# Kernel tuning notes

Measured on AMD Instinct MI355X. Metric: run time of the kernel, lower is better.

## Reference

```python
import jax, jax.numpy as jnp
import numpy as np

N = 100000
E = 1600000
D_IN = 128
D_H = 128
D_OUT = 128
LN_EPS = 1e-5
NORM_EPS = 1e-12


def _sage_conv(x, src, dst, Wl, bl, Wr):
    # PyG SAGEConv(mean): out = lin_l(mean_{j in N(i)} x_j) + lin_r(x_i)
    msgs = x[src]                                             # [E, d] gather
    summed = jax.ops.segment_sum(msgs, dst, num_segments=N)   # [N, d]
    cnt = jax.ops.segment_sum(jnp.ones((src.shape[0],), x.dtype), dst, num_segments=N)
    mean = summed / jnp.maximum(cnt, 1.0)[:, None]
    return mean @ Wl + bl + x @ Wr


def _layer_norm(x, g, b):
    mu = jnp.mean(x, axis=-1, keepdims=True)
    var = jnp.mean(jnp.square(x - mu), axis=-1, keepdims=True)
    return (x - mu) * jax.lax.rsqrt(var + LN_EPS) * g + b


def setup_inputs() -> dict:
    key = jax.random.key(0)
    ks = jax.random.split(key, 20)
    x = jax.random.normal(ks[0], (N, D_IN), dtype=jnp.float32)
    edge_index = jax.random.randint(ks[1], (2, E), 0, N, dtype=jnp.int64)
    dims = [(D_IN, D_H), (D_H, D_H), (D_H, D_OUT)]
    inp = {"x": x, "edge_index": edge_index}
    for i, (di, do) in enumerate(dims):
        s = 1.0 / np.sqrt(di)
        inp[f"Wl{i}"] = jax.random.normal(ks[2 + 5 * i], (di, do), dtype=jnp.float32) * s
        inp[f"bl{i}"] = jnp.zeros((do,), dtype=jnp.float32)
        inp[f"Wr{i}"] = jax.random.normal(ks[3 + 5 * i], (di, do), dtype=jnp.float32) * s
        inp[f"g{i}"] = jnp.ones((do,), dtype=jnp.float32)
        inp[f"b{i}"] = jnp.zeros((do,), dtype=jnp.float32)
    return inp


def reference(x, edge_index, Wl0, bl0, Wr0, g0, b0, Wl1, bl1, Wr1, g1, b1, Wl2, bl2, Wr2, g2, b2):
    src, dst = edge_index[0], edge_index[1]
    params = [(Wl0, bl0, Wr0, g0, b0), (Wl1, bl1, Wr1, g1, b1), (Wl2, bl2, Wr2, g2, b2)]
    h = x
    for i, (Wl, bl, Wr, g, b) in enumerate(params):
        h = _sage_conv(h, src, dst, Wl, bl, Wr)
        h = _layer_norm(h, g, b)
        if i < len(params) - 1:
            h = jax.nn.elu(h)
            # dropout is identity in eval mode
    # F.normalize(p=2, dim=-1)
    nrm = jnp.sqrt(jnp.sum(jnp.square(h), axis=-1, keepdims=True))
    return h / jnp.maximum(nrm, NORM_EPS)
```

## Files before the change

kernel.cpp:

```cpp
#include <hip/hip_runtime.h>
#include <hip/hip_bf16.h>
#include <math.h>

#define N_NODES 100000
#define N_EDGES 1600000
#define D 128
#define NB 391
#define BSTRIDE 6000

#define OFF_SSRC 0
#define OFF_OFFS 6400000
#define OFF_PACK 6800016
#define OFF_GC   7193232
#define OFF_BB   7195296
#define OFF_M    7204112
#define OFF_XHI  58404112
#define OFF_XLO  84004112

typedef __attribute__((ext_vector_type(8))) short short8;
typedef __attribute__((ext_vector_type(4))) float floatx4;

__device__ __forceinline__ unsigned short f2bf(float f) {
    unsigned int u = __float_as_uint(f);
    u += 0x7fffu + ((u >> 16) & 1u);
    return (unsigned short)(u >> 16);
}
__device__ __forceinline__ float bf2f(unsigned short h) {
    return __uint_as_float(((unsigned int)h) << 16);
}

__global__ __launch_bounds__(256) void part_kernel(const int* __restrict__ src,
                                                   const int* __restrict__ dst,
                                                   int* __restrict__ gcur,
                                                   uint2* __restrict__ staging) {
    __shared__ int hist[NB];
    __shared__ int base[NB];
    int t = threadIdx.x;
    int e0 = blockIdx.x * 4096;
    for (int i = t; i < NB; i += 256) hist[i] = 0;
    __syncthreads();
    int d[16];
#pragma unroll
    for (int i = 0; i < 16; ++i) {
        int e = e0 + i * 256 + t;
        d[i] = (e < N_EDGES) ? dst[e] : -1;
        if (d[i] >= 0) atomicAdd(&hist[d[i] >> 8], 1);
    }
    __syncthreads();
    for (int i = t; i < NB; i += 256) {
        int h = hist[i];
        base[i] = h ? atomicAdd(&gcur[i], h) : 0;
    }
    __syncthreads();
    for (int i = t; i < NB; i += 256) hist[i] = 0;
    __syncthreads();
#pragma unroll
    for (int i = 0; i < 16; ++i) {
        if (d[i] >= 0) {
            int e = e0 + i * 256 + t;
            int b = d[i] >> 8;
            int slot = atomicAdd(&hist[b], 1);
            staging[b * BSTRIDE + base[b] + slot] =
                make_uint2((unsigned)src[e], (unsigned)(d[i] & 255));
        }
    }
}

__global__ void bscan_kernel(const int* __restrict__ gcur, int* __restrict__ bbase,
                             int* __restrict__ offs) {
    __shared__ int sh[512];
    int t = threadIdx.x;
    int v = (t < NB) ? gcur[t] : 0;
    sh[t] = v;
    __syncthreads();
    for (int off = 1; off < 512; off <<= 1) {
        int y = (t >= off) ? sh[t - off] : 0;
        __syncthreads();
        sh[t] += y;
        __syncthreads();
    }
    if (t < NB) bbase[t] = sh[t] - v;
    if (t == 0) offs[N_NODES] = N_EDGES;
}

__global__ __launch_bounds__(256) void bsort_kernel(const uint2* __restrict__ staging,
                                                    const int* __restrict__ gcur,
                                                    const int* __restrict__ bbase,
                                                    int* __restrict__ offs,
                                                    int* __restrict__ s_src) {
    __shared__ int cnt[256];
    __shared__ int scn[256];
    __shared__ int ssrc[BSTRIDE];
    int b = blockIdx.x;
    int t = threadIdx.x;
    int n = gcur[b];
    int base_out = bbase[b];
    cnt[t] = 0;
    __syncthreads();
    for (int e = t; e < n; e += 256) {
        uint2 v = staging[b * BSTRIDE + e];
        atomicAdd(&cnt[v.y], 1);
    }
    __syncthreads();
    int v = cnt[t];
    scn[t] = v;
    __syncthreads();
    for (int off = 1; off < 256; off <<= 1) {
        int y = (t >= off) ? scn[t - off] : 0;
        __syncthreads();
        scn[t] += y;
        __syncthreads();
    }
    int ex = scn[t] - v;
    int node = b * 256 + t;
    if (node < N_NODES) offs[node] = base_out + ex;
    cnt[t] = ex;
    __syncthreads();
    for (int e = t; e < n; e += 256) {
        uint2 w = staging[b * BSTRIDE + e];
        int slot = atomicAdd(&cnt[w.y], 1);
        ssrc[slot] = (int)w.x;
    }
    __syncthreads();
    for (int e = t; e < n; e += 256) s_src[base_out + e] = ssrc[e];
}

__global__ void pack_kernel(const float* __restrict__ Wl0, const float* __restrict__ Wr0,
                            const float* __restrict__ Wl1, const float* __restrict__ Wr1,
                            const float* __restrict__ Wl2, const float* __restrict__ Wr2,
                            unsigned short* __restrict__ pack) {
    int tid = blockIdx.x * blockDim.x + threadIdx.x;
    int l = tid >> 15;
    int r = tid & 32767;
    int k = r >> 7;
    int n = r & 127;
    const float* Wl = (l == 0) ? Wl0 : (l == 1) ? Wl1 : Wl2;
    const float* Wr = (l == 0) ? Wr0 : (l == 1) ? Wr1 : Wr2;
    float v = (k < 128) ? Wl[k * 128 + n] : Wr[(k - 128) * 128 + n];
    unsigned short hi = f2bf(v);
    unsigned short lo = f2bf(v - bf2f(hi));
    int ct = n >> 4, ks = k >> 5, lane = ((k >> 3) & 3) * 16 + (n & 15), j = k & 7;
    int idx = ((ct * 8 + ks) * 64 + lane) * 8 + j;
    pack[l * 65536 + idx] = hi;
    pack[l * 65536 + 32768 + idx] = lo;
}

__global__ __launch_bounds__(256) void cvt_kernel(const float* __restrict__ x,
                                                  unsigned int* __restrict__ Xhi,
                                                  unsigned int* __restrict__ Xlo) {
    int i = blockIdx.x * 256 + threadIdx.x;
    float2 v = ((const float2*)x)[i];
    unsigned short h0 = f2bf(v.x), h1 = f2bf(v.y);
    unsigned short l0 = f2bf(v.x - bf2f(h0)), l1 = f2bf(v.y - bf2f(h1));
    Xhi[i] = (unsigned int)h0 | ((unsigned int)h1 << 16);
    Xlo[i] = (unsigned int)l0 | ((unsigned int)l1 << 16);
}

__global__ __launch_bounds__(128, 5) void fused_kernel(const uint4* __restrict__ X4,
                                                       const unsigned short* __restrict__ Xh,
                                                       const unsigned short* __restrict__ Xl,
                                                       unsigned short* __restrict__ XhO,
                                                       unsigned short* __restrict__ XlO,
                                                       const int* __restrict__ s_src,
                                                       const int* __restrict__ offs,
                                                       const unsigned short* __restrict__ packh,
                                                       const unsigned short* __restrict__ packl,
                                                       const float* __restrict__ bl,
                                                       const float* __restrict__ g,
                                                       const float* __restrict__ b,
                                                       float* __restrict__ outf, int last) {
    __shared__ float lmean[32 * 128];
    int t = threadIdx.x;
    int wid = t >> 6, lane = t & 63;
    int sub = lane >> 4, li = lane & 15;
    int nodebase = blockIdx.x * 32;

    int off_l = offs[min(nodebase + wid * 16 + min(lane, 16), N_NODES)];

#define ACC_U4(u)                                                                  \
    do {                                                                           \
        const unsigned int w_[4] = {(u).x, (u).y, (u).z, (u).w};                   \
        _Pragma("unroll") for (int j_ = 0; j_ < 4; ++j_) {                         \
            acc[2 * j_]     += bf2f((unsigned short)w_[j_]);                       \
            acc[2 * j_ + 1] += bf2f((unsigned short)(w_[j_] >> 16));               \
        }                                                                          \
    } while (0)

    for (int i = 0; i < 16; ++i) {
        int lrow = wid * 16 + i;
        int beg = __shfl(off_l, i);
        int end = __shfl(off_l, i + 1);
        int deg = end - beg;
        float acc[8];
#pragma unroll
        for (int j = 0; j < 8; ++j) acc[j] = 0.f;

        for (int cbase = 0; cbase < deg; cbase += 64) {
            int cnt = min(deg - cbase, 64);
            int myidx = s_src[min(beg + cbase + lane, N_EDGES - 1)];
            int j = 0;
            for (; j + 16 <= cnt; j += 16) {
                int i0 = __shfl(myidx, j + sub);
                int i1 = __shfl(myidx, j + 4 + sub);
                int i2 = __shfl(myidx, j + 8 + sub);
                int i3 = __shfl(myidx, j + 12 + sub);
                uint4 u0 = X4[i0 * 16 + li];
                uint4 u1 = X4[i1 * 16 + li];
                uint4 u2 = X4[i2 * 16 + li];
                uint4 u3 = X4[i3 * 16 + li];
                ACC_U4(u0); ACC_U4(u1); ACC_U4(u2); ACC_U4(u3);
            }
            if (j + 8 <= cnt) {
                int i0 = __shfl(myidx, j + sub);
                int i1 = __shfl(myidx, j + 4 + sub);
                uint4 u0 = X4[i0 * 16 + li];
                uint4 u1 = X4[i1 * 16 + li];
                ACC_U4(u0); ACC_U4(u1);
                j += 8;
            }
            if (j + 4 <= cnt) {
                int i0 = __shfl(myidx, j + sub);
                uint4 u0 = X4[i0 * 16 + li];
                ACC_U4(u0);
                j += 4;
            }
            int rem = cnt - j;
            if (rem > 0) {
                int i0 = __shfl(myidx, j + min(sub, rem - 1));
                uint4 u0 = X4[i0 * 16 + li];
                if (sub < rem) ACC_U4(u0);
            }
        }
#pragma unroll
        for (int j = 0; j < 8; ++j) {
            acc[j] += __shfl_xor(acc[j], 16);
            acc[j] += __shfl_xor(acc[j], 32);
        }
        float inv = 1.0f / fmaxf((float)deg, 1.0f);
        if (sub < 2) {
            int chunk = li * 2 + sub;
            floatx4 v = {acc[sub * 4] * inv, acc[sub * 4 + 1] * inv,
                         acc[sub * 4 + 2] * inv, acc[sub * 4 + 3] * inv};
            *(floatx4*)&lmean[lrow * 128 + ((chunk ^ (lrow & 7)) << 2)] = v;
        }
    }
#undef ACC_U4

    int colb = lane & 15;
    int quad = lane >> 4;
    int kq = quad * 8;
    int tilebase = nodebase + wid * 16;

    int rowA = min(tilebase + colb, N_NODES - 1);
    int lrowA = wid * 16 + colb;
    int rsalt = lrowA & 7;

    floatx4 acc[8];
#pragma unroll
    for (int ct = 0; ct < 8; ++ct) acc[ct] = (floatx4){0.f, 0.f, 0.f, 0.f};

#pragma unroll
    for (int ks = 0; ks < 4; ++ks) {
        int chunk0 = ks * 8 + quad * 2;
        short8 ah, al;
        {
            floatx4 v0 = *(const floatx4*)&lmean[lrowA * 128 + ((chunk0 ^ rsalt) << 2)];
            floatx4 v1 = *(const floatx4*)&lmean[lrowA * 128 + (((chunk0 + 1) ^ rsalt) << 2)];
            float v[8] = {v0[0], v0[1], v0[2], v0[3], v1[0], v1[1], v1[2], v1[3]};
#pragma unroll
            for (int j = 0; j < 8; ++j) {
                unsigned short hi = f2bf(v[j]);
                ah[j] = (short)hi;
                al[j] = (short)f2bf(v[j] - bf2f(hi));
            }
        }
#pragma unroll
        for (int ct = 0; ct < 8; ++ct) {
            int fo = ((ct * 8 + ks) << 9) + (lane << 3);
            short8 bh = *(const short8*)(packh + fo);
            short8 bo = *(const short8*)(packl + fo);
            acc[ct] = __builtin_amdgcn_mfma_f32_16x16x32_bf16(ah, bh, acc[ct], 0, 0, 0);
            acc[ct] = __builtin_amdgcn_mfma_f32_16x16x32_bf16(al, bh, acc[ct], 0, 0, 0);
            acc[ct] = __builtin_amdgcn_mfma_f32_16x16x32_bf16(ah, bo, acc[ct], 0, 0, 0);
        }
    }
#pragma unroll
    for (int ks = 4; ks < 8; ++ks) {
        int kof = (ks - 4) * 32 + kq;
        long o = (long)rowA * D + kof;
        short8 ah = *(const short8*)(Xh + o);
        short8 al = *(const short8*)(Xl + o);
#pragma unroll
        for (int ct = 0; ct < 8; ++ct) {
            int fo = ((ct * 8 + ks) << 9) + (lane << 3);
            short8 bh = *(const short8*)(packh + fo);
            short8 bo = *(const short8*)(packl + fo);
            acc[ct] = __builtin_amdgcn_mfma_f32_16x16x32_bf16(ah, bh, acc[ct], 0, 0, 0);
            acc[ct] = __builtin_amdgcn_mfma_f32_16x16x32_bf16(al, bh, acc[ct], 0, 0, 0);
            acc[ct] = __builtin_amdgcn_mfma_f32_16x16x32_bf16(ah, bo, acc[ct], 0, 0, 0);
        }
    }

    float bb[8], gg[8], b2[8];
#pragma unroll
    for (int ct = 0; ct < 8; ++ct) {
        bb[ct] = bl[ct * 16 + colb];
        gg[ct] = g[ct * 16 + colb];
        b2[ct] = b[ct * 16 + colb];
    }

#pragma unroll
    for (int ct = 0; ct < 8; ++ct)
#pragma unroll
        for (int e = 0; e < 4; ++e) acc[ct][e] += bb[ct];
    float mu[4], rstd[4];
#pragma unroll
    for (int e = 0; e < 4; ++e) {
        float s = 0.f;
#pragma unroll
        for (int ct = 0; ct < 8; ++ct) s += acc[ct][e];
        s += __shfl_xor(s, 1); s += __shfl_xor(s, 2);
        s += __shfl_xor(s, 4); s += __shfl_xor(s, 8);
        mu[e] = s * (1.0f / 128.0f);
    }
#pragma unroll
    for (int e = 0; e < 4; ++e) {
        float q = 0.f;
#pragma unroll
        for (int ct = 0; ct < 8; ++ct) {
            float d = acc[ct][e] - mu[e];
            q += d * d;
        }
        q += __shfl_xor(q, 1); q += __shfl_xor(q, 2);
        q += __shfl_xor(q, 4); q += __shfl_xor(q, 8);
        rstd[e] = rsqrtf(q * (1.0f / 128.0f) + 1e-5f);
    }
#pragma unroll
    for (int ct = 0; ct < 8; ++ct)
#pragma unroll
        for (int e = 0; e < 4; ++e) {
            float y = (acc[ct][e] - mu[e]) * rstd[e] * gg[ct] + b2[ct];
            if (!last) y = (y > 0.f) ? y : expm1f(y);
            acc[ct][e] = y;
        }
    if (last) {
#pragma unroll
        for (int e = 0; e < 4; ++e) {
            float ss = 0.f;
#pragma unroll
            for (int ct = 0; ct < 8; ++ct) {
                float y = acc[ct][e];
                ss += y * y;
            }
            ss += __shfl_xor(ss, 1); ss += __shfl_xor(ss, 2);
            ss += __shfl_xor(ss, 4); ss += __shfl_xor(ss, 8);
            float inv = 1.0f / fmaxf(sqrtf(ss), 1e-12f);
#pragma unroll
            for (int ct = 0; ct < 8; ++ct) acc[ct][e] *= inv;
        }
#pragma unroll
        for (int e = 0; e < 4; ++e) {
            int row = tilebase + quad * 4 + e;
            if (row < N_NODES) {
#pragma unroll
                for (int ct = 0; ct < 8; ++ct)
                    outf[(long)row * D + ct * 16 + colb] = acc[ct][e];
            }
        }
    } else {
#pragma unroll
        for (int e = 0; e < 4; ++e) {
            int row = tilebase + quad * 4 + e;
            if (row < N_NODES) {
#pragma unroll
                for (int ct = 0; ct < 8; ++ct) {
                    float y = acc[ct][e];
                    unsigned short hh = f2bf(y);
                    unsigned short ll = f2bf(y - bf2f(hh));
                    long o = (long)row * D + ct * 16 + colb;
                    XhO[o] = hh;
                    XlO[o] = ll;
                }
            }
        }
    }
}

extern "C" void kernel_launch(void* const* d_in, const int* in_sizes, int n_in,
                              void* d_out, int out_size, void* d_ws, size_t ws_size,
                              hipStream_t stream) {
    const float* x = (const float*)d_in[0];
    const int* edges = (const int*)d_in[1];
    const int* src = edges;
    const int* dst = edges + N_EDGES;
    const float* Wl[3] = {(const float*)d_in[2], (const float*)d_in[7],  (const float*)d_in[12]};
    const float* bl[3] = {(const float*)d_in[3], (const float*)d_in[8],  (const float*)d_in[13]};
    const float* Wr[3] = {(const float*)d_in[4], (const float*)d_in[9],  (const float*)d_in[14]};
    const float* g[3]  = {(const float*)d_in[5], (const float*)d_in[10], (const float*)d_in[15]};
    const float* b[3]  = {(const float*)d_in[6], (const float*)d_in[11], (const float*)d_in[16]};

    char* ws = (char*)d_ws;
    int* s_src = (int*)(ws + OFF_SSRC);
    int* offs  = (int*)(ws + OFF_OFFS);
    unsigned short* wpack = (unsigned short*)(ws + OFF_PACK);
    int* gcur  = (int*)(ws + OFF_GC);
    int* bbase = (int*)(ws + OFF_BB);
    uint2* staging = (uint2*)(ws + OFF_M);
    unsigned short* XhB = (unsigned short*)(ws + OFF_M);
    unsigned short* XlB = (unsigned short*)(ws + OFF_M + 25600000);
    unsigned short* XhA = (unsigned short*)(ws + OFF_XHI);
    unsigned short* XlA = (unsigned short*)(ws + OFF_XLO);
    float* out = (float*)d_out;

    hipMemsetAsync(gcur, 0, NB * sizeof(int), stream);
    part_kernel<<<(N_EDGES + 4095) / 4096, 256, 0, stream>>>(src, dst, gcur, staging);
    bscan_kernel<<<1, 512, 0, stream>>>(gcur, bbase, offs);
    bsort_kernel<<<NB, 256, 0, stream>>>(staging, gcur, bbase, offs, s_src);
    pack_kernel<<<(3 * 32768) / 256, 256, 0, stream>>>(Wl[0], Wr[0], Wl[1], Wr[1], Wl[2], Wr[2], wpack);
    cvt_kernel<<<(N_NODES * 64) / 256, 256, 0, stream>>>(x, (unsigned int*)XhA, (unsigned int*)XlA);

    const int FB = (N_NODES + 31) / 32;
    unsigned short* ph[3] = {wpack, wpack + 65536, wpack + 131072};

    fused_kernel<<<FB, 128, 0, stream>>>((const uint4*)XhA, XhA, XlA, XhB, XlB,
                                         s_src, offs, ph[0], ph[0] + 32768,
                                         bl[0], g[0], b[0], nullptr, 0);
    fused_kernel<<<FB, 128, 0, stream>>>((const uint4*)XhB, XhB, XlB, XhA, XlA,
                                         s_src, offs, ph[1], ph[1] + 32768,
                                         bl[1], g[1], b[1], nullptr, 0);
    fused_kernel<<<FB, 128, 0, stream>>>((const uint4*)XhA, XhA, XlA, nullptr, nullptr,
                                         s_src, offs, ph[2], ph[2] + 32768,
                                         bl[2], g[2], b[2], out, 1);
}
```

Baseline: 593.2 us.

## Merge partition, weight pack and convert kernels; pack staging entries into one word

```diff
diff --git a/kernel.cpp b/kernel.cpp
--- a/kernel.cpp
+++ b/kernel.cpp
@@ -29,40 +29,72 @@
     return __uint_as_float(((unsigned int)h) << 16);
 }
 
-__global__ __launch_bounds__(256) void part_kernel(const int* __restrict__ src,
+__global__ __launch_bounds__(256) void prep_kernel(const int* __restrict__ src,
                                                    const int* __restrict__ dst,
                                                    int* __restrict__ gcur,
-                                                   uint2* __restrict__ staging) {
-    __shared__ int hist[NB];
-    __shared__ int base[NB];
+                                                   unsigned int* __restrict__ staging,
+                                                   const float* __restrict__ Wl0, const float* __restrict__ Wr0,
+                                                   const float* __restrict__ Wl1, const float* __restrict__ Wr1,
+                                                   const float* __restrict__ Wl2, const float* __restrict__ Wr2,
+                                                   unsigned short* __restrict__ wpack,
+                                                   const float* __restrict__ x,
+                                                   unsigned int* __restrict__ Xhi,
+                                                   unsigned int* __restrict__ Xlo) {
+    int bid = blockIdx.x;
     int t = threadIdx.x;
-    int e0 = blockIdx.x * 4096;
-    for (int i = t; i < NB; i += 256) hist[i] = 0;
-    __syncthreads();
-    int d[16];
-#pragma unroll
-    for (int i = 0; i < 16; ++i) {
-        int e = e0 + i * 256 + t;
-        d[i] = (e < N_EDGES) ? dst[e] : -1;
-        if (d[i] >= 0) atomicAdd(&hist[d[i] >> 8], 1);
-    }
-    __syncthreads();
-    for (int i = t; i < NB; i += 256) {
-        int h = hist[i];
-        base[i] = h ? atomicAdd(&gcur[i], h) : 0;
-    }
-    __syncthreads();
-    for (int i = t; i < NB; i += 256) hist[i] = 0;
-    __syncthreads();
-#pragma unroll
-    for (int i = 0; i < 16; ++i) {
-        if (d[i] >= 0) {
+    if (bid < NB) {
+        __shared__ int hist[NB];
+        __shared__ int base[NB];
+        int e0 = bid * 4096;
+        for (int i = t; i < NB; i += 256) hist[i] = 0;
+        __syncthreads();
+        int d[16];
+#pragma unroll
+        for (int i = 0; i < 16; ++i) {
             int e = e0 + i * 256 + t;
-            int b = d[i] >> 8;
-            int slot = atomicAdd(&hist[b], 1);
-            staging[b * BSTRIDE + base[b] + slot] =
-                make_uint2((unsigned)src[e], (unsigned)(d[i] & 255));
-        }
+            d[i] = (e < N_EDGES) ? dst[e] : -1;
+            if (d[i] >= 0) atomicAdd(&hist[d[i] >> 8], 1);
+        }
+        __syncthreads();
+        for (int i = t; i < NB; i += 256) {
+            int h = hist[i];
+            base[i] = h ? atomicAdd(&gcur[i], h) : 0;
+        }
+        __syncthreads();
+        for (int i = t; i < NB; i += 256) hist[i] = 0;
+        __syncthreads();
+#pragma unroll
+        for (int i = 0; i < 16; ++i) {
+            if (d[i] >= 0) {
+                int e = e0 + i * 256 + t;
+                int b = d[i] >> 8;
+                int slot = atomicAdd(&hist[b], 1);
+                staging[b * BSTRIDE + base[b] + slot] =
+                    ((unsigned int)src[e] << 8) | (unsigned int)(d[i] & 255);
+            }
+        }
+    } else if (bid < NB + 384) {
+        int tid = (bid - NB) * 256 + t;
+        int l = tid >> 15;
+        int r = tid & 32767;
+        int k = r >> 7;
+        int n = r & 127;
+        const float* Wl = (l == 0) ? Wl0 : (l == 1) ? Wl1 : Wl2;
+        const float* Wr = (l == 0) ? Wr0 : (l == 1) ? Wr1 : Wr2;
+        float v = (k < 128) ? Wl[k * 128 + n] : Wr[(k - 128) * 128 + n];
+        unsigned short hi = f2bf(v);
+        unsigned short lo = f2bf(v - bf2f(hi));
+        int ct = n >> 4, ks = k >> 5, lane = ((k >> 3) & 3) * 16 + (n & 15), j = k & 7;
+        int idx = ((ct * 8 + ks) * 64 + lane) * 8 + j;
+        wpack[l * 65536 + idx] = hi;
+        wpack[l * 65536 + 32768 + idx] = lo;
+    } else {
+        int i = (bid - NB - 384) * 256 + t;
+        float2 v = ((const float2*)x)[i];
+        unsigned short h0 = f2bf(v.x), h1 = f2bf(v.y);
+        unsigned short l0 = f2bf(v.x - bf2f(h0)), l1 = f2bf(v.y - bf2f(h1));
+        Xhi[i] = (unsigned int)h0 | ((unsigned int)h1 << 16);
+        Xlo[i] = (unsigned int)l0 | ((unsigned int)l1 << 16);
     }
 }
 
@@ -83,11 +115,11 @@
     if (t == 0) offs[N_NODES] = N_EDGES;
 }
 
-__global__ __launch_bounds__(256) void bsort_kernel(const uint2* __restrict__ staging,
-                                                    const int* __restrict__ gcur,
-                                                    const int* __restrict__ bbase,
-                                                    int* __restrict__ offs,
-                                                    int* __restrict__ s_src) {
+__global__ __launch_bounds__(1024) void bsort_kernel(const unsigned int* __restrict__ staging,
+                                                     const int* __restrict__ gcur,
+                                                     const int* __restrict__ bbase,
+                                                     int* __restrict__ offs,
+                                                     int* __restrict__ s_src) {
     __shared__ int cnt[256];
     __shared__ int scn[256];
     __shared__ int ssrc[BSTRIDE];
@@ -95,65 +127,35 @@
     int t = threadIdx.x;
     int n = gcur[b];
     int base_out = bbase[b];
-    cnt[t] = 0;
-    __syncthreads();
-    for (int e = t; e < n; e += 256) {
-        uint2 v = staging[b * BSTRIDE + e];
-        atomicAdd(&cnt[v.y], 1);
-    }
-    __syncthreads();
-    int v = cnt[t];
-    scn[t] = v;
+    if (t < 256) cnt[t] = 0;
+    __syncthreads();
+    for (int e = t; e < n; e += 1024)
+        atomicAdd(&cnt[staging[b * BSTRIDE + e] & 255u], 1);
+    __syncthreads();
+    int v = 0;
+    if (t < 256) { v = cnt[t]; scn[t] = v; }
     __syncthreads();
     for (int off = 1; off < 256; off <<= 1) {
-        int y = (t >= off) ? scn[t - off] : 0;
-        __syncthreads();
-        scn[t] += y;
-        __syncthreads();
-    }
-    int ex = scn[t] - v;
-    int node = b * 256 + t;
-    if (node < N_NODES) offs[node] = base_out + ex;
-    cnt[t] = ex;
-    __syncthreads();
-    for (int e = t; e < n; e += 256) {
-        uint2 w = staging[b * BSTRIDE + e];
-        int slot = atomicAdd(&cnt[w.y], 1);
-        ssrc[slot] = (int)w.x;
-    }
-    __syncthreads();
-    for (int e = t; e < n; e += 256) s_src[base_out + e] = ssrc[e];
-}
-
-__global__ void pack_kernel(const float* __restrict__ Wl0, const float* __restrict__ Wr0,
-                            const float* __restrict__ Wl1, const float* __restrict__ Wr1,
-                            const float* __restrict__ Wl2, const float* __restrict__ Wr2,
-                            unsigned short* __restrict__ pack) {
-    int tid = blockIdx.x * blockDim.x + threadIdx.x;
-    int l = tid >> 15;
-    int r = tid & 32767;
-    int k = r >> 7;
-    int n = r & 127;
-    const float* Wl = (l == 0) ? Wl0 : (l == 1) ? Wl1 : Wl2;
-    const float* Wr = (l == 0) ? Wr0 : (l == 1) ? Wr1 : Wr2;
-    float v = (k < 128) ? Wl[k * 128 + n] : Wr[(k - 128) * 128 + n];
-    unsigned short hi = f2bf(v);
-    unsigned short lo = f2bf(v - bf2f(hi));
-    int ct = n >> 4, ks = k >> 5, lane = ((k >> 3) & 3) * 16 + (n & 15), j = k & 7;
-    int idx = ((ct * 8 + ks) * 64 + lane) * 8 + j;
-    pack[l * 65536 + idx] = hi;
-    pack[l * 65536 + 32768 + idx] = lo;
-}
-
-__global__ __launch_bounds__(256) void cvt_kernel(const float* __restrict__ x,
-                                                  unsigned int* __restrict__ Xhi,
-                                                  unsigned int* __restrict__ Xlo) {
-    int i = blockIdx.x * 256 + threadIdx.x;
-    float2 v = ((const float2*)x)[i];
-    unsigned short h0 = f2bf(v.x), h1 = f2bf(v.y);
-    unsigned short l0 = f2bf(v.x - bf2f(h0)), l1 = f2bf(v.y - bf2f(h1));
-    Xhi[i] = (unsigned int)h0 | ((unsigned int)h1 << 16);
-    Xlo[i] = (unsigned int)l0 | ((unsigned int)l1 << 16);
+        int y = 0;
+        if (t < 256 && t >= off) y = scn[t - off];
+        __syncthreads();
+        if (t < 256) scn[t] += y;
+        __syncthreads();
+    }
+    if (t < 256) {
+        int ex = scn[t] - v;
+        int node = b * 256 + t;
+        if (node < N_NODES) offs[node] = base_out + ex;
+        cnt[t] = ex;
+    }
+    __syncthreads();
+    for (int e = t; e < n; e += 1024) {
+        unsigned int w = staging[b * BSTRIDE + e];
+        int slot = atomicAdd(&cnt[w & 255u], 1);
+        ssrc[slot] = (int)(w >> 8);
+    }
+    __syncthreads();
+    for (int e = t; e < n; e += 1024) s_src[base_out + e] = ssrc[e];
 }
 
 __global__ __launch_bounds__(128, 5) void fused_kernel(const uint4* __restrict__ X4,
@@ -405,7 +407,7 @@
     unsigned short* wpack = (unsigned short*)(ws + OFF_PACK);
     int* gcur  = (int*)(ws + OFF_GC);
     int* bbase = (int*)(ws + OFF_BB);
-    uint2* staging = (uint2*)(ws + OFF_M);
+    unsigned int* staging = (unsigned int*)(ws + OFF_M);
     unsigned short* XhB = (unsigned short*)(ws + OFF_M);
     unsigned short* XlB = (unsigned short*)(ws + OFF_M + 25600000);
     unsigned short* XhA = (unsigned short*)(ws + OFF_XHI);
@@ -413,11 +415,12 @@
     float* out = (float*)d_out;
 
     hipMemsetAsync(gcur, 0, NB * sizeof(int), stream);
-    part_kernel<<<(N_EDGES + 4095) / 4096, 256, 0, stream>>>(src, dst, gcur, staging);
+    prep_kernel<<<NB + 384 + 25000, 256, 0, stream>>>(src, dst, gcur, staging,
+                                                      Wl[0], Wr[0], Wl[1], Wr[1], Wl[2], Wr[2],
+                                                      wpack, x, (unsigned int*)XhA,
+                                                      (unsigned int*)XlA);
     bscan_kernel<<<1, 512, 0, stream>>>(gcur, bbase, offs);
-    bsort_kernel<<<NB, 256, 0, stream>>>(staging, gcur, bbase, offs, s_src);
-    pack_kernel<<<(3 * 32768) / 256, 256, 0, stream>>>(Wl[0], Wr[0], Wl[1], Wr[1], Wl[2], Wr[2], wpack);
-    cvt_kernel<<<(N_NODES * 64) / 256, 256, 0, stream>>>(x, (unsigned int*)XhA, (unsigned int*)XlA);
+    bsort_kernel<<<NB, 1024, 0, stream>>>(staging, gcur, bbase, offs, s_src);
 
     const int FB = (N_NODES + 31) / 32;
     unsigned short* ph[3] = {wpack, wpack + 65536, wpack + 131072};
```

Measured after the change: 584.8 us, median of 2. About the same (-1.4%).
